# Kernel optimization log

Measured on AMD Instinct MI355X. Metric: run time of the kernel, lower is better.

Reference implementation:

```python
import jax, jax.numpy as jnp
import numpy as np

B, N, C = 16, 1024, 768
E, H, D, K = 8, 192, 4, 2


def setup_inputs() -> dict:
    key = jax.random.key(0)
    ks = jax.random.split(key, 8)
    std = 0.02
    return {
        "x": jax.random.normal(ks[0], (B, N, C), jnp.float32),
        "task_ids": jax.random.randint(ks[1], (B,), 0, D),
        "eps": jax.random.normal(ks[2], (B, N, E), jnp.float32),
        "gate_w": jax.random.normal(ks[3], (D, C, 2 * E), jnp.float32) * std,
        "fc1_w": jax.random.normal(ks[4], (E, H, C), jnp.float32) * std,
        "fc1_b": jnp.zeros((E, H), jnp.float32),
        "fc2_w": jax.random.normal(ks[5], (E, C, H), jnp.float32) * std,
        "fc2_b": jnp.zeros((E, C), jnp.float32),
    }


def reference(x, task_ids, eps, gate_w, fc1_w, fc1_b, fc2_w, fc2_b):
    # per-sample gate selected by domain/task id: [B,N,2E]
    total_w = jnp.einsum("bnc,bce->bne", x, gate_w[task_ids])
    clean_logits, raw_noise = jnp.split(total_w, 2, axis=-1)  # [B,N,E] each
    noise_stddev = jax.nn.softplus(raw_noise) + 0.01
    logits = clean_logits + eps * noise_stddev  # [B,N,E]
    exp_wise_sum = logits.sum(axis=1)  # [B,E]

    top_k_logits, top_k_idx = jax.lax.top_k(exp_wise_sum, K)  # [B,K]
    m1 = top_k_logits.min(axis=1, keepdims=True)
    m2 = top_k_logits.max(axis=1, keepdims=True)
    scaled = (top_k_logits - m1) / (m2 - m1 + 1e-6)
    top_k_gates = jax.nn.softmax(scaled, axis=1)  # [B,K]

    gates_full = jnp.zeros((B, E), x.dtype).at[
        jnp.arange(B)[:, None], top_k_idx
    ].set(top_k_gates)  # [B,E]

    # dense all-expert adapter compute (faithful to original torch.stack)
    h = jnp.einsum("bnc,ehc->benh", x, fc1_w) + fc1_b[None, :, None, :]
    h = jax.nn.gelu(h, approximate=False)
    expert_outs = jnp.einsum("benh,ech->benc", h, fc2_w) + fc2_b[None, :, None, :]

    tot_x = jnp.einsum("be,benc->bnc", gates_full, expert_outs)
    return x + tot_x
```

## Files before the change

### kernel.cpp

```cpp
#include <hip/hip_runtime.h>

#define B_ 16
#define N_ 1024
#define C_ 768
#define E_ 8
#define H_ 192
#define K_ 2

typedef __bf16 bf16x8 __attribute__((ext_vector_type(8)));
typedef float  f32x4  __attribute__((ext_vector_type(4)));

__global__ __launch_bounds__(256) void prep_kernel(
    const float* __restrict__ w1, const float* __restrict__ w2,
    const float* __restrict__ gw,
    __bf16* __restrict__ pw1, __bf16* __restrict__ pw2,
    float* __restrict__ gwT) {
  int idx = blockIdx.x * 256 + threadIdx.x;
  const int nW4 = (E_ * H_ * C_) / 4;
  if (idx >= nW4) return;
  int flat = idx * 4;
  int e = flat / (H_ * C_);
  int r = flat - e * (H_ * C_);

  {
    float4 a = *(const float4*)(w1 + (size_t)flat);
    int n = r / C_;
    int c = r - n * C_;
    size_t o = ((size_t)(e * 24 + (c >> 5)) * 192 + n) * 32 + (c & 31);
    pw1[o + 0] = (__bf16)a.x; pw1[o + 1] = (__bf16)a.y;
    pw1[o + 2] = (__bf16)a.z; pw1[o + 3] = (__bf16)a.w;
  }
  {
    float4 a = *(const float4*)(w2 + (size_t)flat);
    int n = r / H_;
    int h = r - n * H_;
    size_t o = ((size_t)(e * 6 + (h >> 5)) * 768 + n) * 32 + (h & 31);
    pw2[o + 0] = (__bf16)a.x; pw2[o + 1] = (__bf16)a.y;
    pw2[o + 2] = (__bf16)a.z; pw2[o + 3] = (__bf16)a.w;
  }
  if (idx < (4 * 16 * C_) / 4) {
    int f = idx * 4;
    int d = f / (16 * C_);
    int rr = f - d * (16 * C_);
    int j = rr / C_;
    int c = rr - j * C_;
    const float* src = gw + (size_t)d * C_ * 16 + j;
    float4 v;
    v.x = src[(size_t)(c + 0) * 16]; v.y = src[(size_t)(c + 1) * 16];
    v.z = src[(size_t)(c + 2) * 16]; v.w = src[(size_t)(c + 3) * 16];
    *(float4*)(gwT + (size_t)f) = v;
  }
}

__global__ __launch_bounds__(256, 3) void gate_kernel(
    const float* __restrict__ x, const int* __restrict__ task_ids,
    const float* __restrict__ eps, const float* __restrict__ gwT,
    float* __restrict__ sums, float* __restrict__ xsum) {
  const int b = blockIdx.x >> 6;
  const int token0 = (blockIdx.x & 63) * 16;
  const int tid = threadIdx.x;

  __shared__ __align__(16) float xt[16][772];
  __shared__ float sc[16][16];
  __shared__ float red[16][8];

  const float* xbase = x + ((size_t)b * N_ + token0) * C_;
  for (int it = 0; it < 12; ++it) {
    int chunk = it * 256 + tid;
    int row = chunk / 192;
    int col4 = chunk - row * 192;
    float4 v = *(const float4*)(xbase + (size_t)row * C_ + col4 * 4);
    *(float4*)&xt[row][col4 * 4] = v;
  }
  __syncthreads();

  const int t = tid & 15;
  const int j = tid >> 4;
  const int e = j & 7;
  const int half = j >> 3;
  const int task = task_ids[b];
  const float* wrow = gwT + ((size_t)task * 16 + 8 + e) * C_ + half * 384;
  const float* xrow = &xt[t][half * 384];
  float acc = 0.0f;
#pragma unroll 4
  for (int c = 0; c < 384; c += 4) {
    float4 xv = *(const float4*)(xrow + c);
    float4 wv = *(const float4*)(wrow + c);
    acc += xv.x * wv.x + xv.y * wv.y + xv.z * wv.z + xv.w * wv.w;
  }
  sc[t][j] = acc;

#pragma unroll
  for (int cc = 0; cc < 3; ++cc) {
    int col = tid * 3 + cc;
    float s = 0.0f;
#pragma unroll
    for (int tt = 0; tt < 16; ++tt) s += xt[tt][col];
    atomicAdd(&xsum[(size_t)b * C_ + col], s);
  }
  __syncthreads();

  if (tid < 128) {
    int t2 = tid & 15, e2 = tid >> 4;
    float raw = sc[t2][e2] + sc[t2][e2 + 8];
    float sp = (raw > 20.0f) ? raw : log1pf(expf(raw));
    red[t2][e2] = eps[((size_t)b * N_ + token0 + t2) * E_ + e2] * (sp + 0.01f);
  }
  __syncthreads();
  if (tid < 8) {
    float s = 0.0f;
#pragma unroll
    for (int tt = 0; tt < 16; ++tt) s += red[tt][tid];
    atomicAdd(&sums[b * E_ + tid], s);
  }
}

#define SMEM_EXPERT (64 * 776 * 2 + 64 * 200 * 2 + 32)

__global__ __launch_bounds__(512, 2) void expert_kernel(
    const float* __restrict__ x, const __bf16* __restrict__ pw1,
    const __bf16* __restrict__ pw2, const float* __restrict__ fc1_b,
    const float* __restrict__ fc2_b, const float* __restrict__ sums,
    const float* __restrict__ xsum, const float* __restrict__ gwT,
    const int* __restrict__ task_ids, float* __restrict__ out) {
  const int bid = blockIdx.x;
  const int sxc = bid >> 3;
  const int b = (bid & 7) * 2 + (sxc >> 4);
  const int token0 = (sxc & 15) * 64;
  const int tid = threadIdx.x;
  const int wave = tid >> 6;
  const int wm = wave >> 2;
  const int wn = wave & 3;
  const int lane = tid & 63;
  const int ln = lane & 15;
  const int q8 = (lane >> 4) * 8;
  const int q4 = (lane >> 4) * 4;
  const int arow = wm * 32;

  extern __shared__ char smem[];
  __bf16 (*xs)[776] = reinterpret_cast<__bf16(*)[776]>(smem);
  __bf16 (*hs)[200] = reinterpret_cast<__bf16(*)[200]>(smem + 99328);
  float* sm_clean = reinterpret_cast<float*>(smem + 99328 + 25600);

  const float* xbase = x + ((size_t)b * N_ + token0) * C_;
  for (int it = 0; it < 12; ++it) {
    int chunk = it * 512 + tid;
    int row = chunk / 96;
    int col8 = chunk - row * 96;
    const float* p = xbase + (size_t)row * C_ + col8 * 8;
    float4 v0 = *(const float4*)p;
    float4 v1 = *(const float4*)(p + 4);
    bf16x8 tv;
    tv[0] = (__bf16)v0.x; tv[1] = (__bf16)v0.y; tv[2] = (__bf16)v0.z; tv[3] = (__bf16)v0.w;
    tv[4] = (__bf16)v1.x; tv[5] = (__bf16)v1.y; tv[6] = (__bf16)v1.z; tv[7] = (__bf16)v1.w;
    *(bf16x8*)&xs[row][col8 * 8] = tv;
  }

  {
    const int task = task_ids[b];
    const float* xsb = xsum + (size_t)b * C_;
    const float* gr = gwT + ((size_t)task * 16 + wave) * C_;
    float cl = 0.0f;
#pragma unroll
    for (int c0 = 0; c0 < C_ / 64; ++c0) {
      int c = c0 * 64 + lane;
      cl += xsb[c] * gr[c];
    }
#pragma unroll
    for (int off = 32; off; off >>= 1) cl += __shfl_down(cl, off);
    if (lane == 0) sm_clean[wave] = cl + sums[b * E_ + wave];
  }
  __syncthreads();

  int e_idx[2]; float gate_v[2];
  {
    float best = -INFINITY, best2 = -INFINITY;
    int i1 = 0, i2 = 0;
#pragma unroll
    for (int e = 0; e < E_; ++e) {
      float v = sm_clean[e];
      if (v > best) { best2 = best; i2 = i1; best = v; i1 = e; }
      else if (v > best2) { best2 = v; i2 = e; }
    }
    float d = best - best2;
    float st = d / (d + 1e-6f);
    float et = expf(st);
    e_idx[0] = i1; gate_v[0] = et / (et + 1.0f);
    e_idx[1] = i2; gate_v[1] = 1.0f / (et + 1.0f);
  }

  f32x4 c2[2][12] = {};

  for (int kx = 0; kx < 2; ++kx) {
    const int e = e_idx[kx];
    const float g = gate_v[kx];

    const __bf16* w1l = pw1 + (size_t)e * (24 * 192 * 32)
                            + (size_t)(wn * 48 + ln) * 32 + q8;
    bf16x8 bq[3][3], aq[3][2];
#pragma unroll
    for (int k0 = 0; k0 < 2; ++k0) {
      const __bf16* nx = w1l + (size_t)k0 * 6144;
#pragma unroll
      for (int jj = 0; jj < 3; ++jj) bq[k0][jj] = *(const bf16x8*)(nx + jj * 512);
      aq[k0][0] = *(const bf16x8*)&xs[arow + ln][k0 * 32 + q8];
      aq[k0][1] = *(const bf16x8*)&xs[arow + 16 + ln][k0 * 32 + q8];
    }
    f32x4 c1[2][3] = {};
#pragma unroll
    for (int kb = 0; kb < 24; ++kb) {
      const int p = kb % 3;
      if (kb < 22) {
        const int kn = kb + 2, pn = kn % 3;
        const __bf16* nx = w1l + (size_t)kn * 6144;
#pragma unroll
        for (int jj = 0; jj < 3; ++jj) bq[pn][jj] = *(const bf16x8*)(nx + jj * 512);
        aq[pn][0] = *(const bf16x8*)&xs[arow + ln][kn * 32 + q8];
        aq[pn][1] = *(const bf16x8*)&xs[arow + 16 + ln][kn * 32 + q8];
      }
#pragma unroll
      for (int jj = 0; jj < 3; ++jj) {
        c1[0][jj] = __builtin_amdgcn_mfma_f32_16x16x32_bf16(aq[p][0], bq[p][jj], c1[0][jj], 0, 0, 0);
        c1[1][jj] = __builtin_amdgcn_mfma_f32_16x16x32_bf16(aq[p][1], bq[p][jj], c1[1][jj], 0, 0, 0);
      }
    }
#pragma unroll
    for (int jj = 0; jj < 3; ++jj) {
      int col = wn * 48 + jj * 16 + ln;
      float b1 = fc1_b[e * H_ + col];
#pragma unroll
      for (int m = 0; m < 2; ++m) {
#pragma unroll
        for (int r = 0; r < 4; ++r) {
          int row = arow + m * 16 + q4 + r;
          float v = c1[m][jj][r] + b1;
          float gl = 0.5f * v * (1.0f + erff(v * 0.70710678118f));
          hs[row][col] = (__bf16)(g * gl);
        }
      }
    }
    __syncthreads();

    const __bf16* w2l = pw2 + (size_t)e * (6 * 768 * 32)
                            + (size_t)(wn * 192 + ln) * 32 + q8;
    bf16x8 bh[3][6], av[2][2];
#pragma unroll
    for (int s0 = 0; s0 < 2; ++s0) {
#pragma unroll
      for (int jj = 0; jj < 6; ++jj)
        bh[s0][jj] = *(const bf16x8*)(w2l + (s0 * 6 + jj) * 512);
    }
    av[0][0] = *(const bf16x8*)&hs[arow + ln][q8];
    av[0][1] = *(const bf16x8*)&hs[arow + 16 + ln][q8];
#pragma unroll
    for (int st = 0; st < 12; ++st) {
      const int kb = st >> 1;
      const int half = st & 1;
      const int p = st % 3;
      if (st < 10) {
        const int s2 = st + 2;
        const int kb2 = s2 >> 1, half2 = s2 & 1, p2 = s2 % 3;
        const __bf16* src = w2l + (size_t)kb2 * 24576;
#pragma unroll
        for (int jj = 0; jj < 6; ++jj)
          bh[p2][jj] = *(const bf16x8*)(src + (half2 * 6 + jj) * 512);
        if (half2 == 0) {
          av[kb2 & 1][0] = *(const bf16x8*)&hs[arow + ln][kb2 * 32 + q8];
          av[kb2 & 1][1] = *(const bf16x8*)&hs[arow + 16 + ln][kb2 * 32 + q8];
        }
      }
#pragma unroll
      for (int jj = 0; jj < 6; ++jj) {
        const int cj = half * 6 + jj;
        c2[0][cj] = __builtin_amdgcn_mfma_f32_16x16x32_bf16(av[kb & 1][0], bh[p][jj], c2[0][cj], 0, 0, 0);
        c2[1][cj] = __builtin_amdgcn_mfma_f32_16x16x32_bf16(av[kb & 1][1], bh[p][jj], c2[1][cj], 0, 0, 0);
      }
    }
    __syncthreads();
  }

  const float* xr = x + ((size_t)b * N_ + token0) * C_;
  float* outr = out + ((size_t)b * N_ + token0) * C_;
#pragma unroll
  for (int jj = 0; jj < 12; ++jj) {
    int col = wn * 192 + jj * 16 + ln;
    float b2t = gate_v[0] * fc2_b[e_idx[0] * C_ + col] +
                gate_v[1] * fc2_b[e_idx[1] * C_ + col];
#pragma unroll
    for (int m = 0; m < 2; ++m) {
#pragma unroll
      for (int r = 0; r < 4; ++r) {
        int row = arow + m * 16 + q4 + r;
        size_t off = (size_t)row * C_ + col;
        outr[off] = xr[off] + c2[m][jj][r] + b2t;
      }
    }
  }
}

extern "C" void kernel_launch(void* const* d_in, const int* in_sizes, int n_in,
                              void* d_out, int out_size, void* d_ws, size_t ws_size,
                              hipStream_t stream) {
  const float* x      = (const float*)d_in[0];
  const int*   task   = (const int*)d_in[1];
  const float* eps    = (const float*)d_in[2];
  const float* gate_w = (const float*)d_in[3];
  const float* fc1_w  = (const float*)d_in[4];
  const float* fc1_b  = (const float*)d_in[5];
  const float* fc2_w  = (const float*)d_in[6];
  const float* fc2_b  = (const float*)d_in[7];
  float* out = (float*)d_out;

  const size_t nW = (size_t)E_ * H_ * C_;
  __bf16* pw1 = (__bf16*)d_ws;
  __bf16* pw2 = pw1 + nW;
  float* gwT  = (float*)((char*)d_ws + 2 * nW * sizeof(__bf16));
  float* sums = gwT + 4 * 16 * C_;
  float* xsum = sums + B_ * E_;

  hipMemsetAsync(sums, 0, (B_ * E_ + B_ * C_) * sizeof(float), stream);
  prep_kernel<<<(nW / 4 + 255) / 256, 256, 0, stream>>>(fc1_w, fc2_w, gate_w,
                                                        pw1, pw2, gwT);
  gate_kernel<<<B_ * 64, 256, 0, stream>>>(x, task, eps, gwT, sums, xsum);

  hipFuncSetAttribute(reinterpret_cast<const void*>(expert_kernel),
                      hipFuncAttributeMaxDynamicSharedMemorySize, SMEM_EXPERT);
  expert_kernel<<<B_ * 16, 512, SMEM_EXPERT, stream>>>(
      x, pw1, pw2, fc1_b, fc2_b, sums, xsum, gwT, task, out);
}
```

Baseline: 210.0 us.

## Fuse gate and expert kernels into one cooperative kernel with grid sync

Merges the separate gate-logit kernel into the expert kernel. Each block computes gate logits for its own 64 tokens while staging x into shared memory, writes per-block partial expert sums, and after a cooperative grid-wide sync reduces them to choose the top-2 experts. This removes the memset, a kernel launch, the second full read of x and the atomics on xsum. The cost is a grid barrier and a requirement that all 256 blocks be co-resident. The gate dot products now run inside the large expert blocks, which could add latency before the expert matmuls begin.

```diff
diff --git a/kernel.cpp b/kernel.cpp
--- a/kernel.cpp
+++ b/kernel.cpp
@@ -1,13 +1,16 @@
 #include <hip/hip_runtime.h>
+#include <hip/hip_cooperative_groups.h>
+
+namespace cg = cooperative_groups;
 
 #define B_ 16
 #define N_ 1024
 #define C_ 768
 #define E_ 8
 #define H_ 192
-#define K_ 2
 
 typedef __bf16 bf16x8 __attribute__((ext_vector_type(8)));
+typedef __bf16 bf16x4 __attribute__((ext_vector_type(4)));
 typedef float  f32x4  __attribute__((ext_vector_type(4)));
 
 __global__ __launch_bounds__(256) void prep_kernel(
@@ -52,77 +55,20 @@
   }
 }
 
-__global__ __launch_bounds__(256, 3) void gate_kernel(
+#define XS_OFF   0
+#define XF_OFF   99328
+#define HS_OFF   99328
+#define SC_OFF   (99328 + 49408)
+#define RED_OFF  (SC_OFF + 2048)
+#define BS_OFF   (RED_OFF + 512)
+#define SMEM_FUSED (BS_OFF + 64)
+
+__global__ __launch_bounds__(512, 2) void fused_kernel(
     const float* __restrict__ x, const int* __restrict__ task_ids,
     const float* __restrict__ eps, const float* __restrict__ gwT,
-    float* __restrict__ sums, float* __restrict__ xsum) {
-  const int b = blockIdx.x >> 6;
-  const int token0 = (blockIdx.x & 63) * 16;
-  const int tid = threadIdx.x;
-
-  __shared__ __align__(16) float xt[16][772];
-  __shared__ float sc[16][16];
-  __shared__ float red[16][8];
-
-  const float* xbase = x + ((size_t)b * N_ + token0) * C_;
-  for (int it = 0; it < 12; ++it) {
-    int chunk = it * 256 + tid;
-    int row = chunk / 192;
-    int col4 = chunk - row * 192;
-    float4 v = *(const float4*)(xbase + (size_t)row * C_ + col4 * 4);
-    *(float4*)&xt[row][col4 * 4] = v;
-  }
-  __syncthreads();
-
-  const int t = tid & 15;
-  const int j = tid >> 4;
-  const int e = j & 7;
-  const int half = j >> 3;
-  const int task = task_ids[b];
-  const float* wrow = gwT + ((size_t)task * 16 + 8 + e) * C_ + half * 384;
-  const float* xrow = &xt[t][half * 384];
-  float acc = 0.0f;
-#pragma unroll 4
-  for (int c = 0; c < 384; c += 4) {
-    float4 xv = *(const float4*)(xrow + c);
-    float4 wv = *(const float4*)(wrow + c);
-    acc += xv.x * wv.x + xv.y * wv.y + xv.z * wv.z + xv.w * wv.w;
-  }
-  sc[t][j] = acc;
-
-#pragma unroll
-  for (int cc = 0; cc < 3; ++cc) {
-    int col = tid * 3 + cc;
-    float s = 0.0f;
-#pragma unroll
-    for (int tt = 0; tt < 16; ++tt) s += xt[tt][col];
-    atomicAdd(&xsum[(size_t)b * C_ + col], s);
-  }
-  __syncthreads();
-
-  if (tid < 128) {
-    int t2 = tid & 15, e2 = tid >> 4;
-    float raw = sc[t2][e2] + sc[t2][e2 + 8];
-    float sp = (raw > 20.0f) ? raw : log1pf(expf(raw));
-    red[t2][e2] = eps[((size_t)b * N_ + token0 + t2) * E_ + e2] * (sp + 0.01f);
-  }
-  __syncthreads();
-  if (tid < 8) {
-    float s = 0.0f;
-#pragma unroll
-    for (int tt = 0; tt < 16; ++tt) s += red[tt][tid];
-    atomicAdd(&sums[b * E_ + tid], s);
-  }
-}
-
-#define SMEM_EXPERT (64 * 776 * 2 + 64 * 200 * 2 + 32)
-
-__global__ __launch_bounds__(512, 2) void expert_kernel(
-    const float* __restrict__ x, const __bf16* __restrict__ pw1,
-    const __bf16* __restrict__ pw2, const float* __restrict__ fc1_b,
-    const float* __restrict__ fc2_b, const float* __restrict__ sums,
-    const float* __restrict__ xsum, const float* __restrict__ gwT,
-    const int* __restrict__ task_ids, float* __restrict__ out) {
+    const __bf16* __restrict__ pw1, const __bf16* __restrict__ pw2,
+    const float* __restrict__ fc1_b, const float* __restrict__ fc2_b,
+    float* __restrict__ psums, float* __restrict__ out) {
   const int bid = blockIdx.x;
   const int sxc = bid >> 3;
   const int b = (bid & 7) * 2 + (sxc >> 4);
@@ -136,39 +82,84 @@
   const int q8 = (lane >> 4) * 8;
   const int q4 = (lane >> 4) * 4;
   const int arow = wm * 32;
+  const int task = task_ids[b];
 
   extern __shared__ char smem[];
-  __bf16 (*xs)[776] = reinterpret_cast<__bf16(*)[776]>(smem);
-  __bf16 (*hs)[200] = reinterpret_cast<__bf16(*)[200]>(smem + 99328);
-  float* sm_clean = reinterpret_cast<float*>(smem + 99328 + 25600);
-
-  const float* xbase = x + ((size_t)b * N_ + token0) * C_;
-  for (int it = 0; it < 12; ++it) {
-    int chunk = it * 512 + tid;
-    int row = chunk / 96;
-    int col8 = chunk - row * 96;
-    const float* p = xbase + (size_t)row * C_ + col8 * 8;
-    float4 v0 = *(const float4*)p;
-    float4 v1 = *(const float4*)(p + 4);
-    bf16x8 tv;
-    tv[0] = (__bf16)v0.x; tv[1] = (__bf16)v0.y; tv[2] = (__bf16)v0.z; tv[3] = (__bf16)v0.w;
-    tv[4] = (__bf16)v1.x; tv[5] = (__bf16)v1.y; tv[6] = (__bf16)v1.z; tv[7] = (__bf16)v1.w;
-    *(bf16x8*)&xs[row][col8 * 8] = tv;
-  }
-
-  {
-    const int task = task_ids[b];
-    const float* xsb = xsum + (size_t)b * C_;
-    const float* gr = gwT + ((size_t)task * 16 + wave) * C_;
-    float cl = 0.0f;
-#pragma unroll
-    for (int c0 = 0; c0 < C_ / 64; ++c0) {
-      int c = c0 * 64 + lane;
-      cl += xsb[c] * gr[c];
-    }
-#pragma unroll
-    for (int off = 32; off; off >>= 1) cl += __shfl_down(cl, off);
-    if (lane == 0) sm_clean[wave] = cl + sums[b * E_ + wave];
+  __bf16 (*xs)[776] = reinterpret_cast<__bf16(*)[776]>(smem + XS_OFF);
+  float  (*xf)[772] = reinterpret_cast<float(*)[772]>(smem + XF_OFF);
+  __bf16 (*hs)[200] = reinterpret_cast<__bf16(*)[200]>(smem + HS_OFF);
+  float (*sc2)[16][2] = reinterpret_cast<float(*)[16][2]>(smem + SC_OFF);
+  float (*red)[8] = reinterpret_cast<float(*)[8]>(smem + RED_OFF);
+  float* bsum = reinterpret_cast<float*>(smem + BS_OFF);
+  float* smc  = bsum + 8;
+
+  if (tid < 8) bsum[tid] = 0.0f;
+
+  for (int g = 0; g < 4; ++g) {
+    const float* xb = x + ((size_t)b * N_ + token0 + g * 16) * C_;
+    for (int it = 0; it < 6; ++it) {
+      int chunk = it * 512 + tid;
+      int row = chunk / 192;
+      int col4 = (chunk - row * 192) * 4;
+      float4 v = *(const float4*)(xb + (size_t)row * C_ + col4);
+      *(float4*)&xf[row][col4] = v;
+    }
+    __syncthreads();
+
+    {
+      int t = tid >> 5, j = (tid >> 1) & 15, hf = tid & 1;
+      const float* wr = gwT + ((size_t)task * 16 + j) * C_ + hf * 384;
+      const float* xr_ = &xf[t][hf * 384];
+      float acc = 0.0f;
+#pragma unroll 4
+      for (int c = 0; c < 384; c += 4) {
+        float4 xv = *(const float4*)(xr_ + c);
+        float4 wv = *(const float4*)(wr + c);
+        acc += xv.x * wv.x + xv.y * wv.y + xv.z * wv.z + xv.w * wv.w;
+      }
+      sc2[t][j][hf] = acc;
+    }
+    for (int it = 0; it < 6; ++it) {
+      int chunk = it * 512 + tid;
+      int row = chunk / 192;
+      int col4 = (chunk - row * 192) * 4;
+      float4 v = *(const float4*)&xf[row][col4];
+      bf16x4 o;
+      o[0] = (__bf16)v.x; o[1] = (__bf16)v.y; o[2] = (__bf16)v.z; o[3] = (__bf16)v.w;
+      *(bf16x4*)&xs[g * 16 + row][col4] = o;
+    }
+    __syncthreads();
+
+    if (tid < 128) {
+      int t = tid >> 3, e = tid & 7;
+      float clean = sc2[t][e][0] + sc2[t][e][1];
+      float raw   = sc2[t][e + 8][0] + sc2[t][e + 8][1];
+      float sp = (raw > 20.0f) ? raw : log1pf(expf(raw));
+      red[t][e] = clean +
+          eps[((size_t)b * N_ + token0 + g * 16 + t) * E_ + e] * (sp + 0.01f);
+    }
+    __syncthreads();
+    if (tid < 8) {
+      float s = bsum[tid];
+#pragma unroll
+      for (int t = 0; t < 16; ++t) s += red[t][tid];
+      bsum[tid] = s;
+    }
+  }
+  __syncthreads();
+  if (tid < 8) psums[bid * 8 + tid] = bsum[tid];
+  __threadfence();
+
+  cg::this_grid().sync();
+
+  if (tid < 8) {
+    float s = 0.0f;
+#pragma unroll
+    for (int tile = 0; tile < 16; ++tile) {
+      int srcbid = (((b & 1) * 16 + tile) << 3) | (b >> 1);
+      s += psums[srcbid * 8 + tid];
+    }
+    smc[tid] = s;
   }
   __syncthreads();
 
@@ -178,7 +169,7 @@
     int i1 = 0, i2 = 0;
 #pragma unroll
     for (int e = 0; e < E_; ++e) {
-      float v = sm_clean[e];
+      float v = smc[e];
       if (v > best) { best2 = best; i2 = i1; best = v; i1 = e; }
       else if (v > best2) { best2 = v; i2 = e; }
     }
@@ -314,17 +305,18 @@
   const size_t nW = (size_t)E_ * H_ * C_;
   __bf16* pw1 = (__bf16*)d_ws;
   __bf16* pw2 = pw1 + nW;
-  float* gwT  = (float*)((char*)d_ws + 2 * nW * sizeof(__bf16));
-  float* sums = gwT + 4 * 16 * C_;
-  float* xsum = sums + B_ * E_;
-
-  hipMemsetAsync(sums, 0, (B_ * E_ + B_ * C_) * sizeof(float), stream);
+  float* gwT   = (float*)((char*)d_ws + 2 * nW * sizeof(__bf16));
+  float* psums = gwT + 4 * 16 * C_;
+
   prep_kernel<<<(nW / 4 + 255) / 256, 256, 0, stream>>>(fc1_w, fc2_w, gate_w,
                                                         pw1, pw2, gwT);
-  gate_kernel<<<B_ * 64, 256, 0, stream>>>(x, task, eps, gwT, sums, xsum);
-
-  hipFuncSetAttribute(reinterpret_cast<const void*>(expert_kernel),
-                      hipFuncAttributeMaxDynamicSharedMemorySize, SMEM_EXPERT);
-  expert_kernel<<<B_ * 16, 512, SMEM_EXPERT, stream>>>(
-      x, pw1, pw2, fc1_b, fc2_b, sums, xsum, gwT, task, out);
+
+  hipFuncSetAttribute(reinterpret_cast<const void*>(fused_kernel),
+                      hipFuncAttributeMaxDynamicSharedMemorySize, SMEM_FUSED);
+  void* args[] = {(void*)&x, (void*)&task, (void*)&eps, (void*)&gwT,
+                  (void*)&pw1, (void*)&pw2, (void*)&fc1_b, (void*)&fc2_b,
+                  (void*)&psums, (void*)&out};
+  hipLaunchCooperativeKernel(reinterpret_cast<void*>(fused_kernel),
+                             dim3(B_ * 16), dim3(512), args, SMEM_FUSED,
+                             stream);
 }
```

Measured after the change: 349.7 us. +66.5%, slower.

## Compute full gate logits per block, drop atomics and memset, deepen MFMA prefetch

Applied to the files above, without the earlier changes.

The gate kernel now computes both clean and noise logits per token directly and writes per-block partial sums to a buffer. This replaces the xsum/sums atomics, the memset and the expert kernel's separate clean-logit dot product. The expert kernel reduces those partials itself, picks the experts, and prefetches the first expert's fc1 weights before the x tile load. Prefetch depth rises to 4 stages in the fc1 loop and 3 in the fc2 loop, issued after the MFMAs. In exchange the gate kernel does twice the dot-product work and the expert kernel uses more registers.

```diff
diff --git a/kernel.cpp b/kernel.cpp
--- a/kernel.cpp
+++ b/kernel.cpp
@@ -5,7 +5,6 @@
 #define C_ 768
 #define E_ 8
 #define H_ 192
-#define K_ 2
 
 typedef __bf16 bf16x8 __attribute__((ext_vector_type(8)));
 typedef float  f32x4  __attribute__((ext_vector_type(4)));
@@ -55,7 +54,7 @@
 __global__ __launch_bounds__(256, 3) void gate_kernel(
     const float* __restrict__ x, const int* __restrict__ task_ids,
     const float* __restrict__ eps, const float* __restrict__ gwT,
-    float* __restrict__ sums, float* __restrict__ xsum) {
+    float* __restrict__ psums) {
   const int b = blockIdx.x >> 6;
   const int token0 = (blockIdx.x & 63) * 16;
   const int tid = threadIdx.x;
@@ -76,42 +75,30 @@
 
   const int t = tid & 15;
   const int j = tid >> 4;
-  const int e = j & 7;
-  const int half = j >> 3;
   const int task = task_ids[b];
-  const float* wrow = gwT + ((size_t)task * 16 + 8 + e) * C_ + half * 384;
-  const float* xrow = &xt[t][half * 384];
+  const float* wrow = gwT + ((size_t)task * 16 + j) * C_;
   float acc = 0.0f;
 #pragma unroll 4
-  for (int c = 0; c < 384; c += 4) {
-    float4 xv = *(const float4*)(xrow + c);
+  for (int c = 0; c < C_; c += 4) {
+    float4 xv = *(const float4*)&xt[t][c];
     float4 wv = *(const float4*)(wrow + c);
     acc += xv.x * wv.x + xv.y * wv.y + xv.z * wv.z + xv.w * wv.w;
   }
   sc[t][j] = acc;
-
-#pragma unroll
-  for (int cc = 0; cc < 3; ++cc) {
-    int col = tid * 3 + cc;
-    float s = 0.0f;
-#pragma unroll
-    for (int tt = 0; tt < 16; ++tt) s += xt[tt][col];
-    atomicAdd(&xsum[(size_t)b * C_ + col], s);
-  }
-  __syncthreads();
-
-  if (tid < 128) {
-    int t2 = tid & 15, e2 = tid >> 4;
-    float raw = sc[t2][e2] + sc[t2][e2 + 8];
+  __syncthreads();
+  if (j < 8) {
+    float clean = sc[t][j];
+    float raw = sc[t][j + 8];
     float sp = (raw > 20.0f) ? raw : log1pf(expf(raw));
-    red[t2][e2] = eps[((size_t)b * N_ + token0 + t2) * E_ + e2] * (sp + 0.01f);
+    red[t][j] = clean +
+        eps[((size_t)b * N_ + token0 + t) * E_ + j] * (sp + 0.01f);
   }
   __syncthreads();
   if (tid < 8) {
     float s = 0.0f;
 #pragma unroll
     for (int tt = 0; tt < 16; ++tt) s += red[tt][tid];
-    atomicAdd(&sums[b * E_ + tid], s);
+    psums[(size_t)blockIdx.x * 8 + tid] = s;
   }
 }
 
@@ -120,9 +107,8 @@
 __global__ __launch_bounds__(512, 2) void expert_kernel(
     const float* __restrict__ x, const __bf16* __restrict__ pw1,
     const __bf16* __restrict__ pw2, const float* __restrict__ fc1_b,
-    const float* __restrict__ fc2_b, const float* __restrict__ sums,
-    const float* __restrict__ xsum, const float* __restrict__ gwT,
-    const int* __restrict__ task_ids, float* __restrict__ out) {
+    const float* __restrict__ fc2_b, const float* __restrict__ psums,
+    float* __restrict__ out) {
   const int bid = blockIdx.x;
   const int sxc = bid >> 3;
   const int b = (bid & 7) * 2 + (sxc >> 4);
@@ -140,7 +126,43 @@
   extern __shared__ char smem[];
   __bf16 (*xs)[776] = reinterpret_cast<__bf16(*)[776]>(smem);
   __bf16 (*hs)[200] = reinterpret_cast<__bf16(*)[200]>(smem + 99328);
-  float* sm_clean = reinterpret_cast<float*>(smem + 99328 + 25600);
+  float* smc = reinterpret_cast<float*>(smem + 99328 + 25600);
+
+  {
+    float v = psums[(((size_t)b << 6) | lane) * 8 + wave];
+#pragma unroll
+    for (int off = 32; off; off >>= 1) v += __shfl_down(v, off);
+    if (lane == 0) smc[wave] = v;
+  }
+  __syncthreads();
+
+  int e_idx[2]; float gate_v[2];
+  {
+    float best = -INFINITY, best2 = -INFINITY;
+    int i1 = 0, i2 = 0;
+#pragma unroll
+    for (int e = 0; e < E_; ++e) {
+      float v = smc[e];
+      if (v > best) { best2 = best; i2 = i1; best = v; i1 = e; }
+      else if (v > best2) { best2 = v; i2 = e; }
+    }
+    float d = best - best2;
+    float st = d / (d + 1e-6f);
+    float et = expf(st);
+    e_idx[0] = i1; gate_v[0] = et / (et + 1.0f);
+    e_idx[1] = i2; gate_v[1] = 1.0f / (et + 1.0f);
+  }
+
+  bf16x8 bq[4][3];
+  {
+    const __bf16* w1l = pw1 + (size_t)e_idx[0] * (24 * 192 * 32)
+                            + (size_t)(wn * 48 + ln) * 32 + q8;
+#pragma unroll
+    for (int k0 = 0; k0 < 4; ++k0)
+#pragma unroll
+      for (int jj = 0; jj < 3; ++jj)
+        bq[k0][jj] = *(const bf16x8*)(w1l + (size_t)k0 * 6144 + jj * 512);
+  }
 
   const float* xbase = x + ((size_t)b * N_ + token0) * C_;
   for (int it = 0; it < 12; ++it) {
@@ -155,39 +177,7 @@
     tv[4] = (__bf16)v1.x; tv[5] = (__bf16)v1.y; tv[6] = (__bf16)v1.z; tv[7] = (__bf16)v1.w;
     *(bf16x8*)&xs[row][col8 * 8] = tv;
   }
-
-  {
-    const int task = task_ids[b];
-    const float* xsb = xsum + (size_t)b * C_;
-    const float* gr = gwT + ((size_t)task * 16 + wave) * C_;
-    float cl = 0.0f;
-#pragma unroll
-    for (int c0 = 0; c0 < C_ / 64; ++c0) {
-      int c = c0 * 64 + lane;
-      cl += xsb[c] * gr[c];
-    }
-#pragma unroll
-    for (int off = 32; off; off >>= 1) cl += __shfl_down(cl, off);
-    if (lane == 0) sm_clean[wave] = cl + sums[b * E_ + wave];
-  }
-  __syncthreads();
-
-  int e_idx[2]; float gate_v[2];
-  {
-    float best = -INFINITY, best2 = -INFINITY;
-    int i1 = 0, i2 = 0;
-#pragma unroll
-    for (int e = 0; e < E_; ++e) {
-      float v = sm_clean[e];
-      if (v > best) { best2 = best; i2 = i1; best = v; i1 = e; }
-      else if (v > best2) { best2 = v; i2 = e; }
-    }
-    float d = best - best2;
-    float st = d / (d + 1e-6f);
-    float et = expf(st);
-    e_idx[0] = i1; gate_v[0] = et / (et + 1.0f);
-    e_idx[1] = i2; gate_v[1] = 1.0f / (et + 1.0f);
-  }
+  __syncthreads();
 
   f32x4 c2[2][12] = {};
 
@@ -197,31 +187,35 @@
 
     const __bf16* w1l = pw1 + (size_t)e * (24 * 192 * 32)
                             + (size_t)(wn * 48 + ln) * 32 + q8;
-    bf16x8 bq[3][3], aq[3][2];
-#pragma unroll
-    for (int k0 = 0; k0 < 2; ++k0) {
-      const __bf16* nx = w1l + (size_t)k0 * 6144;
-#pragma unroll
-      for (int jj = 0; jj < 3; ++jj) bq[k0][jj] = *(const bf16x8*)(nx + jj * 512);
+    if (kx == 1) {
+#pragma unroll
+      for (int k0 = 0; k0 < 4; ++k0)
+#pragma unroll
+        for (int jj = 0; jj < 3; ++jj)
+          bq[k0][jj] = *(const bf16x8*)(w1l + (size_t)k0 * 6144 + jj * 512);
+    }
+    bf16x8 aq[4][2];
+#pragma unroll
+    for (int k0 = 0; k0 < 4; ++k0) {
       aq[k0][0] = *(const bf16x8*)&xs[arow + ln][k0 * 32 + q8];
       aq[k0][1] = *(const bf16x8*)&xs[arow + 16 + ln][k0 * 32 + q8];
     }
     f32x4 c1[2][3] = {};
 #pragma unroll
     for (int kb = 0; kb < 24; ++kb) {
-      const int p = kb % 3;
-      if (kb < 22) {
-        const int kn = kb + 2, pn = kn % 3;
-        const __bf16* nx = w1l + (size_t)kn * 6144;
-#pragma unroll
-        for (int jj = 0; jj < 3; ++jj) bq[pn][jj] = *(const bf16x8*)(nx + jj * 512);
-        aq[pn][0] = *(const bf16x8*)&xs[arow + ln][kn * 32 + q8];
-        aq[pn][1] = *(const bf16x8*)&xs[arow + 16 + ln][kn * 32 + q8];
-      }
+      const int p = kb & 3;
 #pragma unroll
       for (int jj = 0; jj < 3; ++jj) {
         c1[0][jj] = __builtin_amdgcn_mfma_f32_16x16x32_bf16(aq[p][0], bq[p][jj], c1[0][jj], 0, 0, 0);
         c1[1][jj] = __builtin_amdgcn_mfma_f32_16x16x32_bf16(aq[p][1], bq[p][jj], c1[1][jj], 0, 0, 0);
+      }
+      if (kb < 20) {
+        const int kn = kb + 4;
+        const __bf16* nx = w1l + (size_t)kn * 6144;
+#pragma unroll
+        for (int jj = 0; jj < 3; ++jj) bq[p][jj] = *(const bf16x8*)(nx + jj * 512);
+        aq[p][0] = *(const bf16x8*)&xs[arow + ln][kn * 32 + q8];
+        aq[p][1] = *(const bf16x8*)&xs[arow + 16 + ln][kn * 32 + q8];
       }
     }
 #pragma unroll
@@ -243,37 +237,41 @@
 
     const __bf16* w2l = pw2 + (size_t)e * (6 * 768 * 32)
                             + (size_t)(wn * 192 + ln) * 32 + q8;
-    bf16x8 bh[3][6], av[2][2];
-#pragma unroll
-    for (int s0 = 0; s0 < 2; ++s0) {
+    bf16x8 bh[3][6], av[3][2];
+#pragma unroll
+    for (int s0 = 0; s0 < 3; ++s0) {
+      const __bf16* src = w2l + (size_t)(s0 >> 1) * 24576;
 #pragma unroll
       for (int jj = 0; jj < 6; ++jj)
-        bh[s0][jj] = *(const bf16x8*)(w2l + (s0 * 6 + jj) * 512);
+        bh[s0][jj] = *(const bf16x8*)(src + ((s0 & 1) * 6 + jj) * 512);
     }
     av[0][0] = *(const bf16x8*)&hs[arow + ln][q8];
     av[0][1] = *(const bf16x8*)&hs[arow + 16 + ln][q8];
+    av[1][0] = *(const bf16x8*)&hs[arow + ln][32 + q8];
+    av[1][1] = *(const bf16x8*)&hs[arow + 16 + ln][32 + q8];
 #pragma unroll
     for (int st = 0; st < 12; ++st) {
       const int kb = st >> 1;
       const int half = st & 1;
       const int p = st % 3;
-      if (st < 10) {
-        const int s2 = st + 2;
-        const int kb2 = s2 >> 1, half2 = s2 & 1, p2 = s2 % 3;
-        const __bf16* src = w2l + (size_t)kb2 * 24576;
-#pragma unroll
-        for (int jj = 0; jj < 6; ++jj)
-          bh[p2][jj] = *(const bf16x8*)(src + (half2 * 6 + jj) * 512);
-        if (half2 == 0) {
-          av[kb2 & 1][0] = *(const bf16x8*)&hs[arow + ln][kb2 * 32 + q8];
-          av[kb2 & 1][1] = *(const bf16x8*)&hs[arow + 16 + ln][kb2 * 32 + q8];
-        }
-      }
+      const int as = kb % 3;
 #pragma unroll
       for (int jj = 0; jj < 6; ++jj) {
         const int cj = half * 6 + jj;
-        c2[0][cj] = __builtin_amdgcn_mfma_f32_16x16x32_bf16(av[kb & 1][0], bh[p][jj], c2[0][cj], 0, 0, 0);
-        c2[1][cj] = __builtin_amdgcn_mfma_f32_16x16x32_bf16(av[kb & 1][1], bh[p][jj], c2[1][cj], 0, 0, 0);
+        c2[0][cj] = __builtin_amdgcn_mfma_f32_16x16x32_bf16(av[as][0], bh[p][jj], c2[0][cj], 0, 0, 0);
+        c2[1][cj] = __builtin_amdgcn_mfma_f32_16x16x32_bf16(av[as][1], bh[p][jj], c2[1][cj], 0, 0, 0);
+      }
+      if (st < 9) {
+        const int s2 = st + 3;
+        const int kb2 = s2 >> 1, half2 = s2 & 1;
+        const __bf16* src = w2l + (size_t)kb2 * 24576;
+#pragma unroll
+        for (int jj = 0; jj < 6; ++jj)
+          bh[p][jj] = *(const bf16x8*)(src + (half2 * 6 + jj) * 512);
+        if (half2 == 0) {
+          av[kb2 % 3][0] = *(const bf16x8*)&hs[arow + ln][kb2 * 32 + q8];
+          av[kb2 % 3][1] = *(const bf16x8*)&hs[arow + 16 + ln][kb2 * 32 + q8];
+        }
       }
     }
     __syncthreads();
@@ -314,17 +312,15 @@
   const size_t nW = (size_t)E_ * H_ * C_;
   __bf16* pw1 = (__bf16*)d_ws;
   __bf16* pw2 = pw1 + nW;
-  float* gwT  = (float*)((char*)d_ws + 2 * nW * sizeof(__bf16));
-  float* sums = gwT + 4 * 16 * C_;
-  float* xsum = sums + B_ * E_;
-
-  hipMemsetAsync(sums, 0, (B_ * E_ + B_ * C_) * sizeof(float), stream);
+  float* gwT   = (float*)((char*)d_ws + 2 * nW * sizeof(__bf16));
+  float* psums = gwT + 4 * 16 * C_;
+
   prep_kernel<<<(nW / 4 + 255) / 256, 256, 0, stream>>>(fc1_w, fc2_w, gate_w,
                                                         pw1, pw2, gwT);
-  gate_kernel<<<B_ * 64, 256, 0, stream>>>(x, task, eps, gwT, sums, xsum);
+  gate_kernel<<<B_ * 64, 256, 0, stream>>>(x, task, eps, gwT, psums);
 
   hipFuncSetAttribute(reinterpret_cast<const void*>(expert_kernel),
                       hipFuncAttributeMaxDynamicSharedMemorySize, SMEM_EXPERT);
   expert_kernel<<<B_ * 16, 512, SMEM_EXPERT, stream>>>(
-      x, pw1, pw2, fc1_b, fc2_b, sums, xsum, gwT, task, out);
+      x, pw1, pw2, fc1_b, fc2_b, psums, out);
 }
```

Result: no change. 206.0 us (-1.9%).
